# Kernel optimization log

Hardware: AMD Instinct MI355X
Metric: run time of the kernel (lower is better)

Reference implementation:

```python
import jax, jax.numpy as jnp
import numpy as np

B, S, D, H, WINDOW = 2, 2048, 2048, 16, 256
HD = D // H  # head_dim = 128

def setup_inputs() -> dict:
    key = jax.random.key(0)
    ks = jax.random.split(key, 6)
    s = 0.02  # initializer_range-like scale for weights
    return {
        "hidden_states": jax.random.normal(ks[0], (B, S, D), jnp.float32),
        "attention_mask": jnp.ones((B, S), jnp.int32),
        "Wq": jax.random.normal(ks[1], (D, D), jnp.float32) * s,
        "Wk": jax.random.normal(ks[2], (D, D), jnp.float32) * s,
        "Wv": jax.random.normal(ks[3], (D, D), jnp.float32) * s,
        "Wo": jax.random.normal(ks[4], (D, D), jnp.float32) * s,
        "bo": jnp.zeros((D,), jnp.float32),
    }

def reference(hidden_states, attention_mask, Wq, Wk, Wv, Wo, bo):
    # GPT-Neo quirk: query is multiplied by sqrt(head_dim) and then
    # dot_product_attention_weights divides by sqrt(head_dim) -> net UNSCALED scores.
    q = (hidden_states @ Wq).reshape(B, S, H, HD)  # [B,S,H,hd]
    k = (hidden_states @ Wk).reshape(B, S, H, HD)
    v = (hidden_states @ Wv).reshape(B, S, H, HD)

    # local causal mask: attend iff i - window < j <= i
    i = jnp.arange(S)[:, None]
    j = jnp.arange(S)[None, :]
    local_causal = (j <= i) & (j > i - WINDOW)  # [S,S]
    mask = local_causal[None, None] & (attention_mask[:, None, None, :] > 0)  # [B,1,S,S]

    neg = jnp.finfo(jnp.float32).min
    scores = jnp.einsum("bqhd,bkhd->bhqk", q, k)  # [B,H,S,S] unscaled
    scores = jnp.where(mask, scores, neg)
    attn = jax.nn.softmax(scores, axis=-1)

    out = jnp.einsum("bhqk,bkhd->bqhd", attn, v).reshape(B, S, D)
    return out @ Wo + bo
```

## Files before the change

kernel.cpp:

```cpp
#include <hip/hip_runtime.h>

#define B_   2
#define S_   2048
#define D_   2048
#define H_   16
#define HD_  128
#define WIN_ 256
#define M_   (B_ * S_)

typedef float  f32x4  __attribute__((ext_vector_type(4)));
typedef short  s16x8  __attribute__((ext_vector_type(8)));
typedef __bf16 bf16x8 __attribute__((ext_vector_type(8)));
typedef unsigned short ushort_t;

__device__ inline unsigned short f2b(float f) {
  unsigned u = __builtin_bit_cast(unsigned, f);
  u += 0x7fffu + ((u >> 16) & 1u);
  return (unsigned short)(u >> 16);
}
__device__ inline float b2f(unsigned short h) {
  unsigned u = ((unsigned)h) << 16;
  return __builtin_bit_cast(float, u);
}

template <typename T>
__device__ auto mfma_impl(T a, T b, f32x4 c, int)
    -> decltype(__builtin_amdgcn_mfma_f32_16x16x32_bf16(a, b, c, 0, 0, 0)) {
  return __builtin_amdgcn_mfma_f32_16x16x32_bf16(a, b, c, 0, 0, 0);
}
template <typename T>
__device__ f32x4 mfma_impl(T a, T b, f32x4 c, long) {
  return __builtin_amdgcn_mfma_f32_16x16x32_bf16(
      __builtin_bit_cast(bf16x8, a), __builtin_bit_cast(bf16x8, b), c, 0, 0, 0);
}
__device__ inline f32x4 mfma_bf16(s16x8 a, s16x8 b, f32x4 c) {
  return mfma_impl(a, b, c, 0);
}

#if defined(__has_builtin)
#if __has_builtin(__builtin_amdgcn_global_load_lds)
#define HAS_GLL 1
#endif
#endif
#ifndef HAS_GLL
#define HAS_GLL 0
#endif

__device__ inline void gl_lds16(const ushort_t* g, ushort_t* lds_wave_base) {
#if HAS_GLL
  __builtin_amdgcn_global_load_lds(
      (const __attribute__((address_space(1))) unsigned int*)g,
      (__attribute__((address_space(3))) unsigned int*)lds_wave_base, 16, 0, 0);
#else
  const int lane = threadIdx.x & 63;
  *(uint4*)(lds_wave_base + lane * 8) = *(const uint4*)g;
#endif
}

__global__ __launch_bounds__(256) void k_split(const float* __restrict__ x,
                                               ushort_t* __restrict__ hi,
                                               ushort_t* __restrict__ lo, int n) {
  int i = (blockIdx.x * 256 + threadIdx.x) * 4;
  if (i + 3 < n) {
    float4 v = *(const float4*)(x + i);
    ushort4 h, l;
    h.x = f2b(v.x); l.x = f2b(v.x - b2f(h.x));
    h.y = f2b(v.y); l.y = f2b(v.y - b2f(h.y));
    h.z = f2b(v.z); l.z = f2b(v.z - b2f(h.z));
    h.w = f2b(v.w); l.w = f2b(v.w - b2f(h.w));
    *(ushort4*)(hi + i) = h;
    *(ushort4*)(lo + i) = l;
  }
}

__global__ __launch_bounds__(256) void k_transpose4(const float* __restrict__ W0,
                                                    const float* __restrict__ W1,
                                                    const float* __restrict__ W2,
                                                    const float* __restrict__ W3,
                                                    ushort_t* __restrict__ T0h,
                                                    ushort_t* __restrict__ T0l,
                                                    ushort_t* __restrict__ T1h,
                                                    ushort_t* __restrict__ T1l,
                                                    ushort_t* __restrict__ T2h,
                                                    ushort_t* __restrict__ T3h) {
  __shared__ float t[32][33];
  const int z = blockIdx.z;
  const float* W = (z == 0) ? W0 : (z == 1) ? W1 : (z == 2) ? W2 : W3;
  ushort_t* Th = (z == 0) ? T0h : (z == 1) ? T1h : (z == 2) ? T2h : T3h;
  ushort_t* Tl = (z == 0) ? T0l : (z == 1) ? T1l : nullptr;
  int bx = blockIdx.x * 32, by = blockIdx.y * 32;
  int tx = threadIdx.x, ty = threadIdx.y;
#pragma unroll
  for (int r = 0; r < 32; r += 8)
    t[ty + r][tx] = W[(size_t)(by + ty + r) * D_ + bx + tx];
  __syncthreads();
#pragma unroll
  for (int r = 0; r < 32; r += 8) {
    float v = t[tx][ty + r];
    unsigned short h = f2b(v);
    Th[(size_t)(bx + ty + r) * D_ + by + tx] = h;
    if (Tl) Tl[(size_t)(bx + ty + r) * D_ + by + tx] = f2b(v - b2f(h));
  }
}

__global__ __launch_bounds__(256) void k_vtrans(const ushort_t* __restrict__ Vb,
                                                ushort_t* __restrict__ Vt) {
  __shared__ ushort_t t[32][33];
  int bx = blockIdx.x * 32, by = blockIdx.y * 32, b = blockIdx.z;
  int tx = threadIdx.x, ty = threadIdx.y;
#pragma unroll
  for (int r = 0; r < 32; r += 8)
    t[ty + r][tx] = Vb[((size_t)(b * S_ + by + ty + r)) * D_ + bx + tx];
  __syncthreads();
#pragma unroll
  for (int r = 0; r < 32; r += 8)
    Vt[((size_t)(b * D_ + bx + ty + r)) * S_ + by + tx] = t[tx][ty + r];
}


__device__ inline void stage_chunk(const ushort_t* __restrict__ gbase, int K,
                                   int rowbase, ushort_t* ldsTile, int tid) {
  const int rr = tid >> 3;
  const int gs = ((tid & 7) ^ (rr & 7)) * 8;
  gl_lds16(gbase + (size_t)(rowbase + rr) * K + gs,
           ldsTile + rowbase * 64 + (tid >> 6) * 512);
}

template <int NSEG, int OUT>
__global__ __launch_bounds__(512) void k_gemm8(
    const ushort_t* __restrict__ A0, const ushort_t* __restrict__ A1,
    const ushort_t* __restrict__ A2, const ushort_t* __restrict__ B0,
    const ushort_t* __restrict__ B2, ushort_t* __restrict__ Co,
    ushort_t* __restrict__ Col, float* __restrict__ Cf,
    const float* __restrict__ bias, int M, int N, int K) {
  __shared__ ushort_t As_[3][256 * 64];
  __shared__ ushort_t Bs_[3][128 * 64];
  const int tid = threadIdx.x;
  const int wave = tid >> 6, lane = tid & 63;
  const int quad = lane >> 4, l16 = lane & 15;
  const int m0 = blockIdx.y * 256, n0 = blockIdx.x * 128;
  const int wrM = (wave >> 1) * 64;
  const int wcN = (wave & 1) * 64;
  const int aRowB = (wrM + l16) * 64;
  const int bRowB = (wcN + l16) * 64;
  int ks8[2];
  ks8[0] = ((0 + quad) ^ (l16 & 7)) * 8;
  ks8[1] = ((4 + quad) ^ (l16 & 7)) * 8;
  const int NT = NSEG * 32;

  {
    const ushort_t* Ab0 = A0 + (size_t)m0 * K;
    const ushort_t* Bb0 = B0 + (size_t)n0 * K;
#pragma unroll
    for (int t = 0; t < 2; ++t) {
      const ushort_t* Ab = Ab0 + t * 64;
      const ushort_t* Bb = Bb0 + t * 64;
      stage_chunk(Ab, K, 0,   &As_[t][0], tid);
      stage_chunk(Ab, K, 64,  &As_[t][0], tid);
      stage_chunk(Ab, K, 128, &As_[t][0], tid);
      stage_chunk(Ab, K, 192, &As_[t][0], tid);
      stage_chunk(Bb, K, 0,   &Bs_[t][0], tid);
      stage_chunk(Bb, K, 64,  &Bs_[t][0], tid);
    }
  }
  asm volatile("s_waitcnt vmcnt(6)" ::: "memory");
  __builtin_amdgcn_s_barrier();
  asm volatile("" ::: "memory");

  f32x4 acc[4][4] = {};
  int cur = 0;
  for (int kt = 0; kt < NT; ++kt) {
    const int st = kt + 2;
    const bool doStage = (st < NT);
    int sbuf = cur + 2; if (sbuf >= 3) sbuf -= 3;
    ushort_t* At  = &As_[cur][0];
    ushort_t* Bt  = &Bs_[cur][0];
    ushort_t* Ads = &As_[sbuf][0];
    ushort_t* Bds = &Bs_[sbuf][0];
    const ushort_t* Asb = A0;
    const ushort_t* Bsb = B0;
    if (doStage) {
      const int sg = st >> 5;
      const ushort_t* Ag = A0;
      const ushort_t* Bg = B0;
      if (NSEG >= 2 && sg == 1) Ag = A1;
      if (NSEG == 3 && sg == 2) { Ag = A2; Bg = B2; }
      Asb = Ag + (size_t)m0 * K + (size_t)(st & 31) * 64;
      Bsb = Bg + (size_t)n0 * K + (size_t)(st & 31) * 64;
    }
    s16x8 bf[4][2];
#pragma unroll
    for (int p = 0; p < 2; ++p) {
      s16x8 af[2][2];
#pragma unroll
      for (int i = 0; i < 2; ++i)
#pragma unroll
        for (int s = 0; s < 2; ++s)
          af[i][s] = *(const s16x8*)(At + aRowB + (p * 2 + i) * 1024 + ks8[s]);
      if (p == 0) {
#pragma unroll
        for (int nt = 0; nt < 4; ++nt)
#pragma unroll
          for (int s = 0; s < 2; ++s)
            bf[nt][s] = *(const s16x8*)(Bt + bRowB + nt * 1024 + ks8[s]);
      }
      if (doStage) {
        if (p == 0) {
          stage_chunk(Asb, K, 0,   Ads, tid);
          stage_chunk(Asb, K, 64,  Ads, tid);
          stage_chunk(Asb, K, 128, Ads, tid);
        } else {
          stage_chunk(Asb, K, 192, Ads, tid);
          stage_chunk(Bsb, K, 0,   Bds, tid);
          stage_chunk(Bsb, K, 64,  Bds, tid);
        }
      }
      __builtin_amdgcn_s_barrier();
      asm volatile("s_waitcnt lgkmcnt(0)" ::: "memory");
      __builtin_amdgcn_sched_barrier(0);
      __builtin_amdgcn_s_setprio(1);
#pragma unroll
      for (int i = 0; i < 2; ++i)
#pragma unroll
        for (int nt = 0; nt < 4; ++nt)
#pragma unroll
          for (int s = 0; s < 2; ++s)
            acc[p * 2 + i][nt] = mfma_bf16(af[i][s], bf[nt][s], acc[p * 2 + i][nt]);
      __builtin_amdgcn_s_setprio(0);
      if (p == 1) {
        if (doStage) asm volatile("s_waitcnt vmcnt(6)" ::: "memory");
        else         asm volatile("s_waitcnt vmcnt(0)" ::: "memory");
      }
      __builtin_amdgcn_s_barrier();
      asm volatile("" ::: "memory");
    }
    cur = (cur == 2) ? 0 : cur + 1;
  }

#pragma unroll
  for (int mt = 0; mt < 4; ++mt)
#pragma unroll
    for (int nt = 0; nt < 4; ++nt)
#pragma unroll
      for (int r = 0; r < 4; ++r) {
        int row = m0 + wrM + mt * 16 + quad * 4 + r;
        int col = n0 + wcN + nt * 16 + l16;
        float v = acc[mt][nt][r];
        if (OUT == 2) {
          Cf[(size_t)row * N + col] = v + bias[col];
        } else if (OUT == 1) {
          unsigned short h = f2b(v);
          Co[(size_t)row * N + col]  = h;
          Col[(size_t)row * N + col] = f2b(v - b2f(h));
        } else {
          Co[(size_t)row * N + col] = f2b(v);
        }
      }
}

__global__ __launch_bounds__(256) void k_fattn(const ushort_t* __restrict__ Qh,
                                               const ushort_t* __restrict__ Ql,
                                               const ushort_t* __restrict__ Kh,
                                               const ushort_t* __restrict__ Vt,
                                               const int* __restrict__ amask,
                                               ushort_t* __restrict__ AO) {
  __shared__ ushort_t Ksh[64][136];
  __shared__ ushort_t Vs[128][72];
  __shared__ ushort_t ps[4][16][72];
  __shared__ int ams[320];
  const int tid = threadIdx.x;
  const int wave = tid >> 6, lane = tid & 63;
  const int quad = lane >> 4, l16 = lane & 15;
  const int qt = blockIdx.x, h = blockIdx.y, b = blockIdx.z;
  const int q0 = qt * 64;

  for (int x = tid; x < 320; x += 256) {
    int j = q0 - 256 + x;
    ams[x] = (j >= 0) ? amask[b * S_ + j] : 0;
  }

  const int qrowA = q0 + wave * 16 + l16;
  const ushort_t* qbh = Qh + ((size_t)(b * S_ + qrowA) * D_) + h * HD_;
  const ushort_t* qbl = Ql + ((size_t)(b * S_ + qrowA) * D_) + h * HD_;
  s16x8 qh[4], ql[4];
#pragma unroll
  for (int kk = 0; kk < 4; kk++) {
    qh[kk] = *(const s16x8*)(qbh + kk * 32 + quad * 8);
    ql[kk] = *(const s16x8*)(qbl + kk * 32 + quad * 8);
  }

  f32x4 O[8] = {};
  float m_run[4], l_run[4];
#pragma unroll
  for (int r = 0; r < 4; r++) { m_run[r] = -3.0e38f; l_run[r] = 0.f; }

  const int t0 = (qt < 4) ? (4 - qt) : 0;
  for (int t = t0; t < 5; t++) {
    const int kb = q0 - 256 + 64 * t;
    __syncthreads();
    {
      const int key = tid >> 2, dimb = (tid & 3) * 32;
      const ushort_t* kgh = Kh + ((size_t)(b * S_ + kb + key) * D_) + h * HD_ + dimb;
#pragma unroll
      for (int u = 0; u < 4; u++)
        *(uint4*)&Ksh[key][dimb + u * 8] = *(const uint4*)(kgh + u * 8);
      const int hd = tid >> 1, keyb = (tid & 1) * 32;
      const ushort_t* vg = Vt + ((size_t)(b * D_ + h * HD_ + hd) * S_) + kb + keyb;
#pragma unroll
      for (int u = 0; u < 4; u++)
        *(uint4*)&Vs[hd][keyb + u * 8] = *(const uint4*)(vg + u * 8);
    }
    __syncthreads();

    f32x4 sacc[4] = {};
#pragma unroll
    for (int kk = 0; kk < 4; kk++)
#pragma unroll
      for (int nt = 0; nt < 4; nt++) {
        s16x8 kfh = *(const s16x8*)&Ksh[nt * 16 + l16][kk * 32 + quad * 8];
        sacc[nt] = mfma_bf16(qh[kk], kfh, sacc[nt]);
        sacc[nt] = mfma_bf16(ql[kk], kfh, sacc[nt]);
      }

#pragma unroll
    for (int nt = 0; nt < 4; nt++) {
      const int j = kb + nt * 16 + l16;
      const bool amok = ams[64 * t + nt * 16 + l16] != 0;
#pragma unroll
      for (int r = 0; r < 4; r++) {
        const int iq = q0 + wave * 16 + quad * 4 + r;
        const bool ok = amok && (j <= iq) && (j > iq - WIN_);
        if (!ok) sacc[nt][r] = -3.0e38f;
      }
    }
    float mt[4];
#pragma unroll
    for (int r = 0; r < 4; r++) {
      mt[r] = fmaxf(fmaxf(sacc[0][r], sacc[1][r]), fmaxf(sacc[2][r], sacc[3][r]));
      mt[r] = fmaxf(mt[r], __shfl_xor(mt[r], 1));
      mt[r] = fmaxf(mt[r], __shfl_xor(mt[r], 2));
      mt[r] = fmaxf(mt[r], __shfl_xor(mt[r], 4));
      mt[r] = fmaxf(mt[r], __shfl_xor(mt[r], 8));
    }
    float alpha[4], lt[4];
#pragma unroll
    for (int r = 0; r < 4; r++) {
      float mnew = fmaxf(m_run[r], mt[r]);
      alpha[r] = __expf(m_run[r] - mnew);
      m_run[r] = mnew;
      lt[r] = 0.f;
#pragma unroll
      for (int nt = 0; nt < 4; nt++) {
        float s = sacc[nt][r];
        float p = (s > -1.0e30f) ? __expf(s - mnew) : 0.f;
        sacc[nt][r] = p;
        lt[r] += p;
      }
      lt[r] += __shfl_xor(lt[r], 1);
      lt[r] += __shfl_xor(lt[r], 2);
      lt[r] += __shfl_xor(lt[r], 4);
      lt[r] += __shfl_xor(lt[r], 8);
      l_run[r] = l_run[r] * alpha[r] + lt[r];
    }
#pragma unroll
    for (int o = 0; o < 8; o++)
#pragma unroll
      for (int r = 0; r < 4; r++) O[o][r] *= alpha[r];
#pragma unroll
    for (int nt = 0; nt < 4; nt++)
#pragma unroll
      for (int r = 0; r < 4; r++)
        ps[wave][quad * 4 + r][nt * 16 + l16] = f2b(sacc[nt][r]);
    __syncthreads();
#pragma unroll
    for (int kk2 = 0; kk2 < 2; kk2++) {
      s16x8 pf = *(const s16x8*)&ps[wave][l16][kk2 * 32 + quad * 8];
#pragma unroll
      for (int o = 0; o < 8; o++) {
        s16x8 vf = *(const s16x8*)&Vs[o * 16 + l16][kk2 * 32 + quad * 8];
        O[o] = mfma_bf16(pf, vf, O[o]);
      }
    }
  }
#pragma unroll
  for (int r = 0; r < 4; r++) l_run[r] = 1.0f / l_run[r];
#pragma unroll
  for (int o = 0; o < 8; o++)
#pragma unroll
    for (int r = 0; r < 4; r++) {
      int row = q0 + wave * 16 + quad * 4 + r;
      AO[((size_t)(b * S_ + row) * D_) + h * HD_ + o * 16 + l16] = f2b(O[o][r] * l_run[r]);
    }
}

extern "C" void kernel_launch(void* const* d_in, const int* in_sizes, int n_in,
                              void* d_out, int out_size, void* d_ws, size_t ws_size,
                              hipStream_t stream) {
  const float* hs    = (const float*)d_in[0];
  const int*   amask = (const int*)d_in[1];
  const float* Wq    = (const float*)d_in[2];
  const float* Wk    = (const float*)d_in[3];
  const float* Wv    = (const float*)d_in[4];
  const float* Wo    = (const float*)d_in[5];
  const float* bo    = (const float*)d_in[6];
  float* out = (float*)d_out;

  char* p = (char*)d_ws;
  ushort_t* hsHi = (ushort_t*)p; p += (size_t)16 << 20;
  ushort_t* hsLo = (ushort_t*)p; p += (size_t)16 << 20;
  ushort_t* WqTh = (ushort_t*)p; p += (size_t)8 << 20;
  ushort_t* WqTl = (ushort_t*)p; p += (size_t)8 << 20;
  ushort_t* WkTh = (ushort_t*)p; p += (size_t)8 << 20;
  ushort_t* WkTl = (ushort_t*)p; p += (size_t)8 << 20;  (void)WkTl;
  ushort_t* WvTh = (ushort_t*)p; p += (size_t)8 << 20;
  ushort_t* WoTh = (ushort_t*)p; p += (size_t)8 << 20;
  ushort_t* Qhb  = (ushort_t*)p; p += (size_t)16 << 20;
  ushort_t* Qlb  = (ushort_t*)p; p += (size_t)16 << 20;
  ushort_t* Khb  = (ushort_t*)p; p += (size_t)16 << 20;
  ushort_t* Vb   = (ushort_t*)p; p += (size_t)16 << 20;
  ushort_t* Vt   = (ushort_t*)p; p += (size_t)16 << 20;

  k_split<<<M_ * D_ / 1024, 256, 0, stream>>>(hs, hsHi, hsLo, M_ * D_);
  dim3 tb(32, 8), tg4(D_ / 32, D_ / 32, 4);
  k_transpose4<<<tg4, tb, 0, stream>>>(Wq, Wk, Wv, Wo, WqTh, WqTl, WkTh, nullptr, WvTh, WoTh);

  dim3 g8(D_ / 128, M_ / 256);
  k_gemm8<3, 1><<<g8, 512, 0, stream>>>(hsHi, hsLo, hsHi, WqTh, WqTl,
                                        Qhb, Qlb, nullptr, nullptr, M_, D_, D_);
  k_gemm8<2, 0><<<g8, 512, 0, stream>>>(hsHi, hsLo, nullptr, WkTh, nullptr,
                                        Khb, nullptr, nullptr, nullptr, M_, D_, D_);
  k_gemm8<1, 0><<<g8, 512, 0, stream>>>(hsHi, nullptr, nullptr, WvTh, nullptr,
                                        Vb, nullptr, nullptr, nullptr, M_, D_, D_);

  dim3 vg(D_ / 32, S_ / 32, B_);
  k_vtrans<<<vg, tb, 0, stream>>>(Vb, Vt);

  dim3 ag(S_ / 64, H_, B_);
  k_fattn<<<ag, 256, 0, stream>>>(Qhb, Qlb, Khb, Vt, amask, hsHi );

  k_gemm8<1, 2><<<g8, 512, 0, stream>>>(hsHi , nullptr, nullptr, WoTh, nullptr,
                                        nullptr, nullptr, out, bo, M_, D_, D_);
}
```

Before: 462.0 us.

## Fuse Q/K/V projection GEMMs into one launch with 256x256 tiles

Replaces the three separate split-precision projection GEMMs with a single kernel in which each block picks Q, K or V by its column index and runs 3, 2 or 1 K-segments. The new kernel uses 256x256 output tiles with K-chunks of 32, a four-stage LDS ring fed by direct global-to-LDS loads, and a remapped block order for L2 locality. The aim is to remove two launch tails, balance uneven per-projection work inside one grid, and reuse A tiles better. The cost is a larger accumulator register footprint and per-block load imbalance, since Q blocks do three times the work of V blocks.

Result: faster. 441.3 us (-4.5%).

```diff
diff --git a/kernel.cpp b/kernel.cpp
--- a/kernel.cpp
+++ b/kernel.cpp
@@ -117,6 +117,148 @@
     Vt[((size_t)(b * D_ + bx + ty + r)) * S_ + by + tx] = t[tx][ty + r];
 }
 
+
+__device__ inline void stage32(const ushort_t* __restrict__ g, int rowbase,
+                               ushort_t* ldsTile, int tid) {
+  const int rr = tid >> 2;
+  const int gs = ((tid & 3) ^ ((rr >> 1) & 3)) * 8;
+  gl_lds16(g + (size_t)(rowbase + rr) * D_ + gs,
+           ldsTile + rowbase * 32 + (tid >> 6) * 512);
+}
+
+__global__ __launch_bounds__(512) void k_qkv(
+    const ushort_t* __restrict__ Ah, const ushort_t* __restrict__ Al,
+    const ushort_t* __restrict__ WqH, const ushort_t* __restrict__ WqL,
+    const ushort_t* __restrict__ WkH, const ushort_t* __restrict__ WvH,
+    ushort_t* __restrict__ Qh, ushort_t* __restrict__ Ql,
+    ushort_t* __restrict__ Ko, ushort_t* __restrict__ Vo) {
+  __shared__ ushort_t As_[4][256 * 32];
+  __shared__ ushort_t Bs_[4][256 * 32];
+  const int tid = threadIdx.x;
+  const int wave = tid >> 6, lane = tid & 63;
+  const int quad = lane >> 4, l16 = lane & 15;
+
+  const int lid = blockIdx.y * 24 + blockIdx.x;
+  const int nlid = (lid & 7) * 48 + (lid >> 3);
+  const int bx = nlid % 24, by = nlid / 24;
+  const int m0 = by * 256;
+  const int wtype = bx >> 3;
+  const int n0 = (bx & 7) * 256;
+  const int nseg = (wtype == 0) ? 3 : (wtype == 1) ? 2 : 1;
+  const ushort_t* Bh0 = (wtype == 0) ? WqH : (wtype == 1) ? WkH : WvH;
+  const int NT = nseg << 6;
+
+  const int wrM = (wave >> 2) * 128;
+  const int wcN = (wave & 3) * 64;
+  const int koff = (quad ^ ((l16 >> 1) & 3)) * 8;
+
+  {
+    const ushort_t* Ap = Ah + (size_t)m0 * D_;
+    const ushort_t* Bp = Bh0 + (size_t)n0 * D_;
+#pragma unroll
+    for (int t = 0; t < 3; ++t) {
+      stage32(Ap + t * 32, 0,   &As_[t][0], tid);
+      stage32(Ap + t * 32, 128, &As_[t][0], tid);
+      stage32(Bp + t * 32, 0,   &Bs_[t][0], tid);
+      stage32(Bp + t * 32, 128, &Bs_[t][0], tid);
+    }
+  }
+  asm volatile("s_waitcnt vmcnt(8)" ::: "memory");
+  __builtin_amdgcn_s_barrier();
+  asm volatile("" ::: "memory");
+
+  f32x4 acc[8][4] = {};
+  for (int kt = 0; kt < NT; ++kt) {
+    const int st = kt + 3;
+    const bool doSt = (st < NT);
+    const int cur = kt & 3, sb = st & 3;
+    const ushort_t* At = &As_[cur][0];
+    const ushort_t* Bt = &Bs_[cur][0];
+    ushort_t* Ad = &As_[sb][0];
+    ushort_t* Bd = &Bs_[sb][0];
+    const ushort_t* Asrc = Ah;
+    const ushort_t* Bsrc = Bh0;
+    if (doSt) {
+      const int sg = st >> 6, so = (st & 63) * 32;
+      const ushort_t* Ab = (sg == 1) ? Al : Ah;
+      const ushort_t* Bb = (sg == 2) ? WqL : Bh0;
+      Asrc = Ab + (size_t)m0 * D_ + so;
+      Bsrc = Bb + (size_t)n0 * D_ + so;
+    }
+    s16x8 bf[4];
+    {
+      s16x8 af[4];
+#pragma unroll
+      for (int mt = 0; mt < 4; ++mt)
+        af[mt] = *(const s16x8*)(At + (wrM + mt * 16 + l16) * 32 + koff);
+#pragma unroll
+      for (int nt = 0; nt < 4; ++nt)
+        bf[nt] = *(const s16x8*)(Bt + (wcN + nt * 16 + l16) * 32 + koff);
+      if (doSt) {
+        stage32(Asrc, 0,   Ad, tid);
+        stage32(Asrc, 128, Ad, tid);
+      }
+      __builtin_amdgcn_s_barrier();
+      asm volatile("s_waitcnt lgkmcnt(0)" ::: "memory");
+      __builtin_amdgcn_sched_barrier(0);
+      __builtin_amdgcn_s_setprio(1);
+#pragma unroll
+      for (int mt = 0; mt < 4; ++mt)
+#pragma unroll
+        for (int nt = 0; nt < 4; ++nt)
+          acc[mt][nt] = mfma_bf16(af[mt], bf[nt], acc[mt][nt]);
+      __builtin_amdgcn_s_setprio(0);
+      __builtin_amdgcn_s_barrier();
+      asm volatile("" ::: "memory");
+    }
+    {
+      s16x8 af[4];
+#pragma unroll
+      for (int mt = 0; mt < 4; ++mt)
+        af[mt] = *(const s16x8*)(At + (wrM + 64 + mt * 16 + l16) * 32 + koff);
+      if (doSt) {
+        stage32(Bsrc, 0,   Bd, tid);
+        stage32(Bsrc, 128, Bd, tid);
+      }
+      __builtin_amdgcn_s_barrier();
+      asm volatile("s_waitcnt lgkmcnt(0)" ::: "memory");
+      __builtin_amdgcn_sched_barrier(0);
+      __builtin_amdgcn_s_setprio(1);
+#pragma unroll
+      for (int mt = 0; mt < 4; ++mt)
+#pragma unroll
+        for (int nt = 0; nt < 4; ++nt)
+          acc[4 + mt][nt] = mfma_bf16(af[mt], bf[nt], acc[4 + mt][nt]);
+      __builtin_amdgcn_s_setprio(0);
+      if (doSt)              asm volatile("s_waitcnt vmcnt(8)" ::: "memory");
+      else if (kt == NT - 3) asm volatile("s_waitcnt vmcnt(4)" ::: "memory");
+      else if (kt == NT - 2) asm volatile("s_waitcnt vmcnt(0)" ::: "memory");
+      __builtin_amdgcn_s_barrier();
+      asm volatile("" ::: "memory");
+    }
+  }
+
+#pragma unroll
+  for (int a = 0; a < 8; ++a)
+#pragma unroll
+    for (int nt = 0; nt < 4; ++nt)
+#pragma unroll
+      for (int r = 0; r < 4; ++r) {
+        const int row = m0 + wrM + a * 16 + quad * 4 + r;
+        const int col = n0 + wcN + nt * 16 + l16;
+        const float v = acc[a][nt][r];
+        const size_t idx = (size_t)row * D_ + col;
+        if (wtype == 0) {
+          unsigned short h = f2b(v);
+          Qh[idx] = h;
+          Ql[idx] = f2b(v - b2f(h));
+        } else if (wtype == 1) {
+          Ko[idx] = f2b(v);
+        } else {
+          Vo[idx] = f2b(v);
+        }
+      }
+}
 
 __device__ inline void stage_chunk(const ushort_t* __restrict__ gbase, int K,
                                    int rowbase, ushort_t* ldsTile, int tid) {
@@ -424,13 +566,8 @@
   dim3 tb(32, 8), tg4(D_ / 32, D_ / 32, 4);
   k_transpose4<<<tg4, tb, 0, stream>>>(Wq, Wk, Wv, Wo, WqTh, WqTl, WkTh, nullptr, WvTh, WoTh);
 
-  dim3 g8(D_ / 128, M_ / 256);
-  k_gemm8<3, 1><<<g8, 512, 0, stream>>>(hsHi, hsLo, hsHi, WqTh, WqTl,
-                                        Qhb, Qlb, nullptr, nullptr, M_, D_, D_);
-  k_gemm8<2, 0><<<g8, 512, 0, stream>>>(hsHi, hsLo, nullptr, WkTh, nullptr,
-                                        Khb, nullptr, nullptr, nullptr, M_, D_, D_);
-  k_gemm8<1, 0><<<g8, 512, 0, stream>>>(hsHi, nullptr, nullptr, WvTh, nullptr,
-                                        Vb, nullptr, nullptr, nullptr, M_, D_, D_);
+  dim3 gq(24, 16);
+  k_qkv<<<gq, 512, 0, stream>>>(hsHi, hsLo, WqTh, WqTl, WkTh, WvTh, Qhb, Qlb, Khb, Vb);
 
   dim3 vg(D_ / 32, S_ / 32, B_);
   k_vtrans<<<vg, tb, 0, stream>>>(Vb, Vt);
@@ -438,6 +575,7 @@
   dim3 ag(S_ / 64, H_, B_);
   k_fattn<<<ag, 256, 0, stream>>>(Qhb, Qlb, Khb, Vt, amask, hsHi );
 
-  k_gemm8<1, 2><<<g8, 512, 0, stream>>>(hsHi , nullptr, nullptr, WoTh, nullptr,
+  dim3 gg(D_ / 128, M_ / 256);
+  k_gemm8<1, 2><<<gg, 512, 0, stream>>>(hsHi , nullptr, nullptr, WoTh, nullptr,
                                         nullptr, nullptr, out, bo, M_, D_, D_);
 }
```
